# Optimization experiments

Measured on AMD Instinct MI355X. Metric: run time of the kernel, lower is better.

The kernel has to match this reference:

```python
import jax, jax.numpy as jnp
import numpy as np

SIGMA = 0.5   # pairwise density bandwidth (density_std)
EPS = 1e-8
B, N, K, P, D, F, H = 8, 20, 2, 320, 3, 64, 64


def setup_inputs() -> dict:
    key = jax.random.key(0)
    ks = jax.random.split(key, 8)
    # ring graph: neighbor node index for each of the K=2 incident slots
    nbr = np.stack([(np.arange(N) - 1) % N, (np.arange(N) + 1) % N], axis=1).astype(np.int32)
    return {
        "X": jax.random.uniform(ks[0], (B, N, K, P, D), minval=-1.0, maxval=1.0),
        "W": jax.random.uniform(ks[1], (B, N, K, P), minval=0.1, maxval=1.0),
        "feats": jax.random.normal(ks[2], (B, N, F)),
        "mu": 0.1 * jax.random.normal(ks[3], (N, K, D)),
        "W1": jax.random.normal(ks[4], (N, F, H)) / np.sqrt(F),
        "Wx": jax.random.normal(ks[5], (N, D, H)) / np.sqrt(D),
        "b1": jnp.zeros((N, H), jnp.float32),
        "W2": jax.random.normal(ks[6], (N, H)) / np.sqrt(H),
        "bias2": jnp.zeros((N,), jnp.float32),
        "nbr_idx": jnp.asarray(nbr),
    }


def reference(X, W, feats, mu, W1, Wx, b1, W2, bias2, nbr_idx):
    # X: [B,N,K,P,D] belief/message particles, W: [B,N,K,P] particle weights
    Bs, Ns, Ks, Ps, Ds = X.shape
    KP = Ks * Ps
    # normalize incoming message weights per node (as in uniform_init: sum over K*P == 1)
    Wn = W / (W.sum(axis=(2, 3), keepdims=True) + EPS)
    Xf = X.reshape(Bs, Ns, KP, Ds)
    Wf = Wn.reshape(Bs, Ns, KP)
    # irregular gather of each node's neighbors' particles/weights
    Xn = Xf[:, nbr_idx]   # [B,N,K,KP,D]
    Wnb = Wf[:, nbr_idx]  # [B,N,K,KP]
    # pairwise edge density: Gaussian on (x_dst - mu_e) vs x_src, via ||a||^2+||b||^2-2ab
    a = X - mu[None, :, :, None, :]                      # [B,N,K,P,D]
    cross = jnp.einsum('bnkpd,bnkqd->bnkpq', a, Xn)      # [B,N,K,P,KP]
    d2 = (a * a).sum(-1)[..., None] + (Xn * Xn).sum(-1)[..., None, :] - 2.0 * cross
    kern = jnp.exp(-d2 / (2.0 * SIGMA * SIGMA))
    # neighbor message: weighted density sum over neighbor particles
    msg = jnp.einsum('bnkpq,bnkq->bnkp', kern, Wnb)      # [B,N,K,P]
    # per-node unary likelihood MLP on (image features, particle state)
    hf = jnp.einsum('bnf,nfh->bnh', feats, W1)           # [B,N,H]
    hx = jnp.einsum('bnkpd,ndh->bnkph', X, Wx)           # [B,N,K,P,H]
    h = jax.nn.relu(hf[:, :, None, None, :] + hx + b1[None, :, None, None, :])
    u = jax.nn.sigmoid(jnp.einsum('bnkph,nh->bnkp', h, W2) + bias2[None, :, None, None])
    # belief weight update: unary * neighbor message, renormalized per node
    w = u * msg
    return w / (w.sum(axis=(2, 3), keepdims=True) + EPS)
```

## Files before the change

### kernel.cpp

```cpp
#include <hip/hip_runtime.h>

constexpr int B_ = 8, N_ = 20, K_ = 2, P_ = 320, D_ = 3, F_ = 64, H_ = 64;
constexpr int Q_ = K_ * P_;
constexpr float EPS_ = 1e-8f;
constexpr float LOG2E_ = 1.4426950408889634f;
constexpr int TILES_ = 10;
constexpr int ROWS_  = 64;

__global__ __launch_bounds__(256) void main_kernel(
    const float* __restrict__ X,
    const float* __restrict__ W,
    const float* __restrict__ feats,
    const float* __restrict__ mu,
    const float* __restrict__ W1,
    const float* __restrict__ Wx,
    const float* __restrict__ b1,
    const float* __restrict__ W2,
    const float* __restrict__ bias2,
    const int* __restrict__ nbr,
    float* __restrict__ wsPart,
    float* __restrict__ out)
{
    __shared__ float4 sQ[Q_];
    __shared__ float4 aT[ROWS_];
    __shared__ float4 xT[ROWS_];
    __shared__ float4 gT[H_];
    __shared__ float  hbT[H_];
    __shared__ float  part[ROWS_][17];
    __shared__ float  red[4];
    __shared__ float  invW;

    const int blk  = blockIdx.x;
    const int bn   = blk / TILES_;
    const int tile = blk - bn * TILES_;
    const int b    = bn / N_;
    const int n    = bn - b * N_;
    const int tid  = threadIdx.x;
    const int wave = tid >> 6;
    const int lane = tid & 63;
    const int k    = (tile >= 5) ? 1 : 0;
    const int r0   = tile * ROWS_;
    const int j    = nbr[n * 2 + k];

    const size_t nbase = ((size_t)b * N_ + j) * Q_;
    float wsum = 0.f;
    for (int i = tid; i < Q_; i += 256) {
        const float* xp = X + (nbase + i) * D_;
        const float x0 = xp[0], x1 = xp[1], x2 = xp[2];
        const float sq = x0 * x0 + x1 * x1 + x2 * x2;
        const float w  = W[nbase + i];
        const float c  = w * __builtin_amdgcn_exp2f(-2.f * LOG2E_ * sq);
        sQ[i] = make_float4(x0, x1, x2, c);
        wsum += w;
    }
    {
        float v = wsum;
        #pragma unroll
        for (int off = 32; off > 0; off >>= 1) v += __shfl_down(v, off, 64);
        if (lane == 0) red[wave] = v;
    }

    if (tid < ROWS_) {
        const int gr = r0 + tid;
        const float* xp = X + ((size_t)bn * Q_ + gr) * D_;
        const float x0 = xp[0], x1 = xp[1], x2 = xp[2];
        const float* mup = mu + (n * K_ + k) * D_;
        const float a0 = x0 - mup[0];
        const float a1 = x1 - mup[1];
        const float a2 = x2 - mup[2];
        const float ra2 = a0 * a0 + a1 * a1 + a2 * a2;
        aT[tid] = make_float4(a0 * (4.f * LOG2E_), a1 * (4.f * LOG2E_),
                              a2 * (4.f * LOG2E_), -2.f * LOG2E_ * ra2);
        xT[tid] = make_float4(x0, x1, x2, 0.f);

        const int h = tid;
        const float* fp  = feats + (size_t)bn * F_;
        const float* w1p = W1 + (size_t)n * F_ * H_ + h;
        float acc = 0.f;
        #pragma unroll 8
        for (int f = 0; f < F_; ++f)
            acc = fmaf(fp[f], w1p[(size_t)f * H_], acc);
        hbT[h] = acc + b1[n * H_ + h];
        const float* wxp = Wx + (size_t)n * D_ * H_ + h;
        gT[h] = make_float4(wxp[0], wxp[H_], wxp[2 * H_], W2[n * H_ + h]);
    }
    __syncthreads();

    if (tid == 0)
        invW = 1.f / (((red[0] + red[1]) + (red[2] + red[3])) + EPS_);

    const int g = tid >> 4;
    const int s = tid & 15;
    float S0[4], S1[4], S2[4], RA[4], acc[4];
    #pragma unroll
    for (int jj = 0; jj < 4; ++jj) {
        const float4 av = aT[g * 4 + jj];
        S0[jj] = av.x; S1[jj] = av.y; S2[jj] = av.z; RA[jj] = av.w;
        acc[jj] = 0.f;
    }
    #pragma unroll 4
    for (int i = 0; i < Q_ / 16; ++i) {
        const float4 Pq = sQ[i * 16 + s];
        #pragma unroll
        for (int jj = 0; jj < 4; ++jj) {
            const float d = fmaf(Pq.x, S0[jj],
                            fmaf(Pq.y, S1[jj],
                            fmaf(Pq.z, S2[jj], RA[jj])));
            acc[jj] = fmaf(Pq.w, __builtin_amdgcn_exp2f(d), acc[jj]);
        }
    }
    #pragma unroll
    for (int jj = 0; jj < 4; ++jj)
        part[g * 4 + jj][s] = acc[jj];

    __syncthreads();

    if (tid < ROWS_) {
        const int row = tid;
        const float* pr = part[row];
        const float msg =
            (((pr[0] + pr[1]) + (pr[2] + pr[3])) + ((pr[4] + pr[5]) + (pr[6] + pr[7]))) +
            (((pr[8] + pr[9]) + (pr[10] + pr[11])) + ((pr[12] + pr[13]) + (pr[14] + pr[15])));

        const float4 xr = xT[row];
        float accg = bias2[n];
        #pragma unroll 8
        for (int h = 0; h < H_; ++h) {
            const float4 gv = gT[h];
            float t = fmaf(xr.x, gv.x, fmaf(xr.y, gv.y, fmaf(xr.z, gv.z, hbT[h])));
            t = fmaxf(t, 0.f);
            accg = fmaf(t, gv.w, accg);
        }
        const float u = 1.f / (1.f + __expf(-accg));
        const float wval = u * msg * invW;

        out[(size_t)bn * Q_ + r0 + row] = wval;

        float v = wval;
        #pragma unroll
        for (int off = 32; off > 0; off >>= 1) v += __shfl_down(v, off, 64);
        if (tid == 0) wsPart[blk] = v;
    }
}

__global__ __launch_bounds__(Q_) void norm_kernel(
    const float* __restrict__ wsPart, float* __restrict__ out)
{
    const int bn = blockIdx.x;
    const float* p = wsPart + bn * TILES_;
    float s0 = 0.f, s1 = 0.f;
    #pragma unroll
    for (int t = 0; t < TILES_ / 2; ++t) { s0 += p[2 * t]; s1 += p[2 * t + 1]; }
    const float inv = 1.f / ((s0 + s1) + EPS_);
    out[(size_t)bn * Q_ + threadIdx.x] *= inv;
}

extern "C" void kernel_launch(void* const* d_in, const int* in_sizes, int n_in,
                              void* d_out, int out_size, void* d_ws, size_t ws_size,
                              hipStream_t stream) {
    const float* X     = (const float*)d_in[0];
    const float* W     = (const float*)d_in[1];
    const float* feats = (const float*)d_in[2];
    const float* mu    = (const float*)d_in[3];
    const float* W1    = (const float*)d_in[4];
    const float* Wx    = (const float*)d_in[5];
    const float* b1    = (const float*)d_in[6];
    const float* W2    = (const float*)d_in[7];
    const float* bias2 = (const float*)d_in[8];
    const int*   nbr   = (const int*)d_in[9];
    float*       out   = (float*)d_out;
    float*       wsPart = (float*)d_ws;

    main_kernel<<<B_ * N_ * TILES_, 256, 0, stream>>>(
        X, W, feats, mu, W1, Wx, b1, W2, bias2, nbr, wsPart, out);
    norm_kernel<<<B_ * N_, Q_, 0, stream>>>(wsPart, out);
}
```

Before: 91.58 us.

## Pack neighbor particles pairwise and use packed FP32 FMA in pairwise density loop

```diff
diff --git a/kernel.cpp b/kernel.cpp
--- a/kernel.cpp
+++ b/kernel.cpp
@@ -6,6 +6,18 @@
 constexpr float LOG2E_ = 1.4426950408889634f;
 constexpr int TILES_ = 10;
 constexpr int ROWS_  = 64;
+
+typedef float v2f __attribute__((ext_vector_type(2)));
+
+__device__ __forceinline__ v2f mk2(float a, float b) { v2f r; r.x = a; r.y = b; return r; }
+
+__device__ __forceinline__ v2f pfma(v2f a, v2f b, v2f c) {
+#if __has_builtin(__builtin_elementwise_fma)
+    return __builtin_elementwise_fma(a, b, c);
+#else
+    v2f r; r.x = fmaf(a.x, b.x, c.x); r.y = fmaf(a.y, b.y, c.y); return r;
+#endif
+}
 
 __global__ __launch_bounds__(256) void main_kernel(
     const float* __restrict__ X,
@@ -21,12 +33,13 @@
     float* __restrict__ wsPart,
     float* __restrict__ out)
 {
-    __shared__ float4 sQ[Q_];
+    __shared__ float4 sA[P_];
+    __shared__ float4 sB[P_];
     __shared__ float4 aT[ROWS_];
     __shared__ float4 xT[ROWS_];
     __shared__ float4 gT[H_];
     __shared__ float  hbT[H_];
-    __shared__ float  part[ROWS_][17];
+    __shared__ float  part[ROWS_][33];
     __shared__ float  red[4];
     __shared__ float  invW;
 
@@ -50,7 +63,10 @@
         const float sq = x0 * x0 + x1 * x1 + x2 * x2;
         const float w  = W[nbase + i];
         const float c  = w * __builtin_amdgcn_exp2f(-2.f * LOG2E_ * sq);
-        sQ[i] = make_float4(x0, x1, x2, c);
+        const int t = i >> 1, e = i & 1;
+        float* pa = (float*)&sA[t];
+        float* pb = (float*)&sB[t];
+        pa[e] = x0; pa[2 + e] = x1; pb[e] = x2; pb[2 + e] = c;
         wsum += w;
     }
     {
@@ -89,38 +105,47 @@
     if (tid == 0)
         invW = 1.f / (((red[0] + red[1]) + (red[2] + red[3])) + EPS_);
 
-    const int g = tid >> 4;
-    const int s = tid & 15;
-    float S0[4], S1[4], S2[4], RA[4], acc[4];
+    const int g = tid >> 5;
+    const int s = tid & 31;
+    float S0[8], S1[8], S2[8], RA[8];
+    v2f acc[8];
     #pragma unroll
-    for (int jj = 0; jj < 4; ++jj) {
-        const float4 av = aT[g * 4 + jj];
+    for (int jj = 0; jj < 8; ++jj) {
+        const float4 av = aT[g * 8 + jj];
         S0[jj] = av.x; S1[jj] = av.y; S2[jj] = av.z; RA[jj] = av.w;
-        acc[jj] = 0.f;
-    }
-    #pragma unroll 4
-    for (int i = 0; i < Q_ / 16; ++i) {
-        const float4 Pq = sQ[i * 16 + s];
-        #pragma unroll
-        for (int jj = 0; jj < 4; ++jj) {
-            const float d = fmaf(Pq.x, S0[jj],
-                            fmaf(Pq.y, S1[jj],
-                            fmaf(Pq.z, S2[jj], RA[jj])));
-            acc[jj] = fmaf(Pq.w, __builtin_amdgcn_exp2f(d), acc[jj]);
+        acc[jj] = mk2(0.f, 0.f);
+    }
+    #pragma unroll 2
+    for (int i = 0; i < P_ / 32; ++i) {
+        const int pi = i * 32 + s;
+        const float4 A  = sA[pi];
+        const float4 Bv = sB[pi];
+        #pragma unroll
+        for (int jj = 0; jj < 8; ++jj) {
+            const v2f d = pfma(mk2(A.x, A.y), mk2(S0[jj], S0[jj]),
+                          pfma(mk2(A.z, A.w), mk2(S1[jj], S1[jj]),
+                          pfma(mk2(Bv.x, Bv.y), mk2(S2[jj], S2[jj]),
+                               mk2(RA[jj], RA[jj]))));
+            const v2f e = mk2(__builtin_amdgcn_exp2f(d.x),
+                              __builtin_amdgcn_exp2f(d.y));
+            acc[jj] = pfma(mk2(Bv.z, Bv.w), e, acc[jj]);
         }
     }
     #pragma unroll
-    for (int jj = 0; jj < 4; ++jj)
-        part[g * 4 + jj][s] = acc[jj];
+    for (int jj = 0; jj < 8; ++jj)
+        part[g * 8 + jj][s] = acc[jj].x + acc[jj].y;
 
     __syncthreads();
 
     if (tid < ROWS_) {
         const int row = tid;
         const float* pr = part[row];
-        const float msg =
-            (((pr[0] + pr[1]) + (pr[2] + pr[3])) + ((pr[4] + pr[5]) + (pr[6] + pr[7]))) +
-            (((pr[8] + pr[9]) + (pr[10] + pr[11])) + ((pr[12] + pr[13]) + (pr[14] + pr[15])));
+        float m0 = 0.f, m1 = 0.f, m2 = 0.f, m3 = 0.f;
+        #pragma unroll
+        for (int c = 0; c < 32; c += 4) {
+            m0 += pr[c]; m1 += pr[c + 1]; m2 += pr[c + 2]; m3 += pr[c + 3];
+        }
+        const float msg = (m0 + m1) + (m2 + m3);
 
         const float4 xr = xT[row];
         float accg = bias2[n];
```

After: 92.27 us. Within noise of the previous version (+0.8%).

## Spread feature MLP and gate reductions across all four waves; vectorize neighbor loads

Applied to the files above, without the earlier changes.

```diff
diff --git a/kernel.cpp b/kernel.cpp
--- a/kernel.cpp
+++ b/kernel.cpp
@@ -26,6 +26,8 @@
     __shared__ float4 xT[ROWS_];
     __shared__ float4 gT[H_];
     __shared__ float  hbT[H_];
+    __shared__ float  gpart[H_][5];
+    __shared__ float  tgate[ROWS_][5];
     __shared__ float  part[ROWS_][17];
     __shared__ float  red[4];
     __shared__ float  invW;
@@ -44,20 +46,45 @@
 
     const size_t nbase = ((size_t)b * N_ + j) * Q_;
     float wsum = 0.f;
-    for (int i = tid; i < Q_; i += 256) {
-        const float* xp = X + (nbase + i) * D_;
-        const float x0 = xp[0], x1 = xp[1], x2 = xp[2];
-        const float sq = x0 * x0 + x1 * x1 + x2 * x2;
-        const float w  = W[nbase + i];
-        const float c  = w * __builtin_amdgcn_exp2f(-2.f * LOG2E_ * sq);
-        sQ[i] = make_float4(x0, x1, x2, c);
-        wsum += w;
+    if (tid < Q_ / 4) {
+        const int t = tid;
+        const float4* xv = (const float4*)(X + nbase * D_);
+        const float4 f0 = xv[3 * t];
+        const float4 f1 = xv[3 * t + 1];
+        const float4 f2 = xv[3 * t + 2];
+        const float4 w4 = ((const float4*)(W + nbase))[t];
+        const float c0 = w4.x * __builtin_amdgcn_exp2f(-2.f * LOG2E_ *
+                         (f0.x * f0.x + f0.y * f0.y + f0.z * f0.z));
+        const float c1 = w4.y * __builtin_amdgcn_exp2f(-2.f * LOG2E_ *
+                         (f0.w * f0.w + f1.x * f1.x + f1.y * f1.y));
+        const float c2 = w4.z * __builtin_amdgcn_exp2f(-2.f * LOG2E_ *
+                         (f1.z * f1.z + f1.w * f1.w + f2.x * f2.x));
+        const float c3 = w4.w * __builtin_amdgcn_exp2f(-2.f * LOG2E_ *
+                         (f2.y * f2.y + f2.z * f2.z + f2.w * f2.w));
+        sQ[4 * t]     = make_float4(f0.x, f0.y, f0.z, c0);
+        sQ[4 * t + 1] = make_float4(f0.w, f1.x, f1.y, c1);
+        sQ[4 * t + 2] = make_float4(f1.z, f1.w, f2.x, c2);
+        sQ[4 * t + 3] = make_float4(f2.y, f2.z, f2.w, c3);
+        wsum = (w4.x + w4.y) + (w4.z + w4.w);
     }
     {
         float v = wsum;
         #pragma unroll
         for (int off = 32; off > 0; off >>= 1) v += __shfl_down(v, off, 64);
         if (lane == 0) red[wave] = v;
+    }
+
+    {
+        const int h = tid & 63, seg = tid >> 6;
+        const float* fp  = feats + (size_t)bn * F_;
+        const float* w1p = W1 + (size_t)n * F_ * H_ + h;
+        float acc = 0.f;
+        #pragma unroll
+        for (int f = 0; f < 16; ++f) {
+            const int ff = seg * 16 + f;
+            acc = fmaf(fp[ff], w1p[(size_t)ff * H_], acc);
+        }
+        gpart[h][seg] = acc;
     }
 
     if (tid < ROWS_) {
@@ -72,20 +99,14 @@
         aT[tid] = make_float4(a0 * (4.f * LOG2E_), a1 * (4.f * LOG2E_),
                               a2 * (4.f * LOG2E_), -2.f * LOG2E_ * ra2);
         xT[tid] = make_float4(x0, x1, x2, 0.f);
-
-        const int h = tid;
-        const float* fp  = feats + (size_t)bn * F_;
-        const float* w1p = W1 + (size_t)n * F_ * H_ + h;
-        float acc = 0.f;
-        #pragma unroll 8
-        for (int f = 0; f < F_; ++f)
-            acc = fmaf(fp[f], w1p[(size_t)f * H_], acc);
-        hbT[h] = acc + b1[n * H_ + h];
-        const float* wxp = Wx + (size_t)n * D_ * H_ + h;
-        gT[h] = make_float4(wxp[0], wxp[H_], wxp[2 * H_], W2[n * H_ + h]);
+        const float* wxp = Wx + (size_t)n * D_ * H_ + tid;
+        gT[tid] = make_float4(wxp[0], wxp[H_], wxp[2 * H_], W2[n * H_ + tid]);
     }
     __syncthreads();
 
+    if (tid < H_)
+        hbT[tid] = ((gpart[tid][0] + gpart[tid][1]) +
+                    (gpart[tid][2] + gpart[tid][3])) + b1[n * H_ + tid];
     if (tid == 0)
         invW = 1.f / (((red[0] + red[1]) + (red[2] + red[3])) + EPS_);
 
@@ -115,22 +136,30 @@
 
     __syncthreads();
 
+    {
+        const int row = tid & 63, seg = tid >> 6;
+        const float4 xr = xT[row];
+        float accg = 0.f;
+        #pragma unroll
+        for (int hh = 0; hh < 16; ++hh) {
+            const int h = seg * 16 + hh;
+            const float4 gv = gT[h];
+            float t = fmaf(xr.x, gv.x, fmaf(xr.y, gv.y, fmaf(xr.z, gv.z, hbT[h])));
+            t = fmaxf(t, 0.f);
+            accg = fmaf(t, gv.w, accg);
+        }
+        tgate[row][seg] = accg;
+    }
+    __syncthreads();
+
     if (tid < ROWS_) {
         const int row = tid;
         const float* pr = part[row];
         const float msg =
             (((pr[0] + pr[1]) + (pr[2] + pr[3])) + ((pr[4] + pr[5]) + (pr[6] + pr[7]))) +
             (((pr[8] + pr[9]) + (pr[10] + pr[11])) + ((pr[12] + pr[13]) + (pr[14] + pr[15])));
-
-        const float4 xr = xT[row];
-        float accg = bias2[n];
-        #pragma unroll 8
-        for (int h = 0; h < H_; ++h) {
-            const float4 gv = gT[h];
-            float t = fmaf(xr.x, gv.x, fmaf(xr.y, gv.y, fmaf(xr.z, gv.z, hbT[h])));
-            t = fmaxf(t, 0.f);
-            accg = fmaf(t, gv.w, accg);
-        }
+        const float accg = bias2[n] + ((tgate[row][0] + tgate[row][1]) +
+                                       (tgate[row][2] + tgate[row][3]));
         const float u = 1.f / (1.f + __expf(-accg));
         const float wval = u * msg * invW;
 
```

New measurement: 88.71 us. 1.03x faster.
